# Kernel optimization log

Hardware: AMD Instinct MI355X
Metric: run time of the kernel (lower is better)

Reference implementation:

```python
import jax, jax.numpy as jnp
import numpy as np

B, L, D = 8, 2048, 512
H, P = 8, 4
C = D // H  # dim_per_head


def setup_inputs() -> dict:
    key = jax.random.key(0)
    ks = jax.random.split(key, 11)
    sc = lambda k, shape, s=0.02: jax.random.normal(k, shape, jnp.float32) * s
    return dict(
        query=jax.random.normal(ks[0], (B, L, D), jnp.float32),
        key_in=jax.random.normal(ks[1], (B, L, D), jnp.float32),
        value=jax.random.normal(ks[2], (B, L, D), jnp.float32),
        W_v=sc(ks[3], (D, D)), b_v=jnp.zeros((D,), jnp.float32),
        W_off=sc(ks[4], (D, H * P * 2), 0.01), b_off=sc(ks[5], (H * P * 2,), 0.2),
        W_aw=sc(ks[6], (D, H * P), 0.01), b_aw=jnp.zeros((H * P,), jnp.float32),
        W_out=sc(ks[7], (D, D)), b_out=jnp.zeros((D,), jnp.float32),
    )


def reference(query, key_in, value, W_v, b_v, W_off, b_off, W_aw, b_aw, W_out, b_out):
    # value projection
    v = value @ W_v + b_v                                        # (B,L,D)
    # sampling offsets and attention weights from the query
    off = (query @ W_off + b_off).reshape(B, L, H, P, 2)         # (B,L,H,P,2)
    aw = jax.nn.softmax((query @ W_aw + b_aw).reshape(B, L, H, P), axis=-1)
    # reference point for query i is (x=linspace[0]=0, y=linspace[i]) because
    # the torch code slices reference_points[:, :, :, :1, :]
    ref_y = jnp.linspace(0.0, 1.0, L, dtype=jnp.float32)
    loc_x = jnp.clip(off[..., 0], 0.0, 1.0)                      # ref_x = 0
    loc_y = jnp.clip(off[..., 1] + ref_y[None, :, None, None], 0.0, 1.0)
    # grid_sample, align_corners=False, input (BH, C, 1, L)
    ix = ((loc_x + 1.0) * L - 1.0) * 0.5                         # width coord in [ (L-1)/2, L-0.5 ]
    iy = loc_y * 0.5                                             # ((y+1)*1 - 1)/2
    ix0 = jnp.floor(ix)
    fx = ix - ix0
    iy0 = jnp.floor(iy)
    fy = iy - iy0
    # height dim has size 1: row iy0 valid iff ==0, row iy0+1 valid iff ==0 (zero padding)
    ywt = (1.0 - fy) * (iy0 == 0.0).astype(jnp.float32) + fy * ((iy0 + 1.0) == 0.0).astype(jnp.float32)
    i0 = ix0.astype(jnp.int32)
    i1 = i0 + 1

    perm = lambda a: a.transpose(0, 2, 1, 3)                     # (B,L,H,P) -> (B,H,L,P)
    i0p, i1p = perm(i0), perm(i1)
    vh = v.reshape(B, L, H, C).transpose(0, 2, 1, 3)             # (B,H,L,C)

    gather = jax.vmap(jax.vmap(lambda vm, ii: vm[ii]))           # (L,C),(L,P) -> (L,P,C)
    m0 = ((i0p >= 0) & (i0p < L)).astype(jnp.float32)[..., None]
    m1 = ((i1p >= 0) & (i1p < L)).astype(jnp.float32)[..., None]
    g0 = gather(vh, jnp.clip(i0p, 0, L - 1)) * m0                # (B,H,L,P,C)
    g1 = gather(vh, jnp.clip(i1p, 0, L - 1)) * m1

    fxp = perm(fx)[..., None]
    ywtp = perm(ywt)[..., None]
    samp = ywtp * ((1.0 - fxp) * g0 + fxp * g1)                  # (B,H,L,P,C)
    out = (samp * perm(aw)[..., None]).sum(axis=3)               # (B,H,L,C)
    out = out.transpose(0, 2, 1, 3).reshape(B, L, D)
    return out @ W_out + b_out
```

## Files before the change

### kernel.cpp

```cpp
#include <hip/hip_runtime.h>
#include <stdint.h>

#define PSZF (16384 * 96)

using short8  = __attribute__((ext_vector_type(8))) short;
using floatx4 = __attribute__((ext_vector_type(4))) float;

__device__ __forceinline__ unsigned short f2bf(float f) {
  union { float f; unsigned u; } v; v.f = f;
  unsigned r = v.u + 0x7fffu + ((v.u >> 16) & 1u);
  return (unsigned short)(r >> 16);
}
__device__ __forceinline__ float bf2f(unsigned short u) {
  union { unsigned u; float f; } v; v.u = ((unsigned)u) << 16; return v.f;
}

__device__ __forceinline__ void load_lds16(const void* g, void* l) {
  __builtin_amdgcn_global_load_lds(
      (const __attribute__((address_space(1))) unsigned int*)g,
      (__attribute__((address_space(3))) unsigned int*)l, 16, 0, 0);
}

__device__ __forceinline__ short8 cvt8(float4 a, float4 b) {
  short8 r;
  r[0] = (short)f2bf(a.x); r[1] = (short)f2bf(a.y);
  r[2] = (short)f2bf(a.z); r[3] = (short)f2bf(a.w);
  r[4] = (short)f2bf(b.x); r[5] = (short)f2bf(b.y);
  r[6] = (short)f2bf(b.z); r[7] = (short)f2bf(b.w);
  return r;
}

__global__ __launch_bounds__(256) void prep_all(const float* __restrict__ W_v,
                                                const float* __restrict__ W_out,
                                                const float* __restrict__ Woff,
                                                const float* __restrict__ Waw,
                                                unsigned short* __restrict__ Wv_t,
                                                unsigned short* __restrict__ Wo_t,
                                                unsigned short* __restrict__ Bhi,
                                                unsigned short* __restrict__ Blo) {
  int t = blockIdx.x * 256 + threadIdx.x;
  if (t < 262144) {
    int n = t >> 9, k = t & 511;
    Wv_t[t] = f2bf(W_v[(k << 9) + n]);
    return;
  }
  t -= 262144;
  if (t < 262144) {
    int n = t >> 9, k = t & 511;
    Wo_t[t] = f2bf(W_out[(k << 9) + n]);
    return;
  }
  t -= 262144;
  if (t < 49152) {
    int n = t >> 9, k = t & 511;
    float w = (n < 64) ? Woff[(k << 6) + n] : Waw[(k << 5) + (n - 64)];
    unsigned short hi = f2bf(w);
    Bhi[t] = hi;
    Blo[t] = f2bf(w - bf2f(hi));
  }
}

__device__ __forceinline__ void gemm_body64_bf16A(unsigned char* smem,
                                                  const unsigned short* __restrict__ A,
                                                  const unsigned short* __restrict__ Bt,
                                                  const float* __restrict__ bias,
                                                  float* __restrict__ C, int bx, int by) {
  unsigned short* lA = (unsigned short*)smem;
  unsigned short* lB = (unsigned short*)(smem + 16384);
  int tid  = threadIdx.x;
  int lane = tid & 63, wv = tid >> 6;
  int wm = wv & 1, wn = wv >> 1;
  int lrow = lane & 15, quad = lane >> 4;
  int rowBlk = by * 128, colBlk = bx * 128;

  const unsigned short* Ab = A + (size_t)rowBlk * 512;
  const unsigned short* Bb = Bt + (size_t)colBlk * 512;
  int r0 = tid >> 2;
  int c0 = (tid & 3) << 3;

  floatx4 acc[4][4];
#pragma unroll
  for (int i = 0; i < 4; i++)
#pragma unroll
    for (int j = 0; j < 4; j++) acc[i][j] = (floatx4){0.f, 0.f, 0.f, 0.f};

  for (int k0 = 0; k0 < 512; k0 += 64) {
    load_lds16(Ab + (size_t)r0 * 512 + k0 + c0,             lA + tid * 8);
    load_lds16(Ab + (size_t)(r0 + 64) * 512 + k0 + c0,      lA + 2048 + tid * 8);
    load_lds16(Bb + (size_t)r0 * 512 + k0 + c0,             lB + tid * 8);
    load_lds16(Bb + (size_t)(r0 + 64) * 512 + k0 + c0,      lB + 2048 + tid * 8);
    load_lds16(Ab + (size_t)r0 * 512 + k0 + 32 + c0,        lA + 4096 + tid * 8);
    load_lds16(Ab + (size_t)(r0 + 64) * 512 + k0 + 32 + c0, lA + 6144 + tid * 8);
    load_lds16(Bb + (size_t)r0 * 512 + k0 + 32 + c0,        lB + 4096 + tid * 8);
    load_lds16(Bb + (size_t)(r0 + 64) * 512 + k0 + 32 + c0, lB + 6144 + tid * 8);
    __syncthreads();

#pragma unroll
    for (int kc = 0; kc < 2; kc++) {
      short8 a[4], b[4];
#pragma unroll
      for (int mi = 0; mi < 4; mi++)
        a[mi] = *(const short8*)&lA[kc * 4096 + (wm * 64 + mi * 16 + lrow) * 32 + quad * 8];
#pragma unroll
      for (int ni = 0; ni < 4; ni++)
        b[ni] = *(const short8*)&lB[kc * 4096 + (wn * 64 + ni * 16 + lrow) * 32 + quad * 8];
#pragma unroll
      for (int mi = 0; mi < 4; mi++)
#pragma unroll
        for (int ni = 0; ni < 4; ni++)
          acc[mi][ni] = __builtin_amdgcn_mfma_f32_16x16x32_bf16(a[mi], b[ni], acc[mi][ni], 0, 0, 0);
    }
    __syncthreads();
  }

#pragma unroll
  for (int ni = 0; ni < 4; ni++) {
    int col = colBlk + wn * 64 + ni * 16 + lrow;
    float bv = bias[col];
#pragma unroll
    for (int mi = 0; mi < 4; mi++) {
      int row = rowBlk + wm * 64 + mi * 16 + quad * 4;
#pragma unroll
      for (int r = 0; r < 4; r++)
        C[(size_t)(row + r) * 512 + col] = acc[mi][ni][r] + bv;
    }
  }
}

__device__ __forceinline__ void gemm_body64_f32A(unsigned char* smem,
                                                 const float* __restrict__ Af,
                                                 const unsigned short* __restrict__ Bt,
                                                 const float* __restrict__ bias,
                                                 unsigned short* __restrict__ C, int bx, int by) {
  unsigned short* lA = (unsigned short*)smem;
  unsigned short* lB = (unsigned short*)(smem + 16384);
  int tid  = threadIdx.x;
  int lane = tid & 63, wv = tid >> 6;
  int wm = wv & 1, wn = wv >> 1;
  int lrow = lane & 15, quad = lane >> 4;
  int rowBlk = by * 128, colBlk = bx * 128;

  const unsigned short* Bb = Bt + (size_t)colBlk * 512;
  int r0 = tid >> 2;
  int c0 = (tid & 3) << 3;
  const float* Ar0 = Af + (size_t)(rowBlk + r0) * 512 + c0;
  const float* Ar1 = Af + (size_t)(rowBlk + r0 + 64) * 512 + c0;

  floatx4 acc[4][4];
#pragma unroll
  for (int i = 0; i < 4; i++)
#pragma unroll
    for (int j = 0; j < 4; j++) acc[i][j] = (floatx4){0.f, 0.f, 0.f, 0.f};

  float4 a00 = *(const float4*)(Ar0);
  float4 a01 = *(const float4*)(Ar0 + 4);
  float4 a10 = *(const float4*)(Ar1);
  float4 a11 = *(const float4*)(Ar1 + 4);
  float4 a02 = *(const float4*)(Ar0 + 32);
  float4 a03 = *(const float4*)(Ar0 + 36);
  float4 a12 = *(const float4*)(Ar1 + 32);
  float4 a13 = *(const float4*)(Ar1 + 36);

  for (int k0 = 0; k0 < 512; k0 += 64) {
    load_lds16(Bb + (size_t)r0 * 512 + k0 + c0,             lB + tid * 8);
    load_lds16(Bb + (size_t)(r0 + 64) * 512 + k0 + c0,      lB + 2048 + tid * 8);
    load_lds16(Bb + (size_t)r0 * 512 + k0 + 32 + c0,        lB + 4096 + tid * 8);
    load_lds16(Bb + (size_t)(r0 + 64) * 512 + k0 + 32 + c0, lB + 6144 + tid * 8);
    *(short8*)&lA[tid * 8]        = cvt8(a00, a01);
    *(short8*)&lA[2048 + tid * 8] = cvt8(a10, a11);
    *(short8*)&lA[4096 + tid * 8] = cvt8(a02, a03);
    *(short8*)&lA[6144 + tid * 8] = cvt8(a12, a13);
    if (k0 < 448) {
      int kk = k0 + 64;
      a00 = *(const float4*)(Ar0 + kk);
      a01 = *(const float4*)(Ar0 + kk + 4);
      a10 = *(const float4*)(Ar1 + kk);
      a11 = *(const float4*)(Ar1 + kk + 4);
      a02 = *(const float4*)(Ar0 + kk + 32);
      a03 = *(const float4*)(Ar0 + kk + 36);
      a12 = *(const float4*)(Ar1 + kk + 32);
      a13 = *(const float4*)(Ar1 + kk + 36);
      asm volatile("s_waitcnt vmcnt(8)" ::: "memory");
    } else {
      asm volatile("s_waitcnt vmcnt(0)" ::: "memory");
    }
    asm volatile("s_waitcnt lgkmcnt(0)" ::: "memory");
    __builtin_amdgcn_sched_barrier(0);
    __builtin_amdgcn_s_barrier();
    __builtin_amdgcn_sched_barrier(0);

#pragma unroll
    for (int kc = 0; kc < 2; kc++) {
      short8 a[4], b[4];
#pragma unroll
      for (int mi = 0; mi < 4; mi++)
        a[mi] = *(const short8*)&lA[kc * 4096 + (wm * 64 + mi * 16 + lrow) * 32 + quad * 8];
#pragma unroll
      for (int ni = 0; ni < 4; ni++)
        b[ni] = *(const short8*)&lB[kc * 4096 + (wn * 64 + ni * 16 + lrow) * 32 + quad * 8];
#pragma unroll
      for (int mi = 0; mi < 4; mi++)
#pragma unroll
        for (int ni = 0; ni < 4; ni++)
          acc[mi][ni] = __builtin_amdgcn_mfma_f32_16x16x32_bf16(a[mi], b[ni], acc[mi][ni], 0, 0, 0);
    }
    __builtin_amdgcn_sched_barrier(0);
    __builtin_amdgcn_s_barrier();
  }

#pragma unroll
  for (int ni = 0; ni < 4; ni++) {
    int col = colBlk + wn * 64 + ni * 16 + lrow;
    float bv = bias[col];
#pragma unroll
    for (int mi = 0; mi < 4; mi++) {
      int row = rowBlk + wm * 64 + mi * 16 + quad * 4;
#pragma unroll
      for (int r = 0; r < 4; r++)
        C[(size_t)(row + r) * 512 + col] = f2bf(acc[mi][ni][r] + bv);
    }
  }
}

__device__ __forceinline__ void swz512(int bid, int& bx, int& by) {
  int x = bid & 7, s = bid >> 3;
  by = (x << 4) | (s >> 2);
  bx = s & 3;
}

__device__ __forceinline__ void offaw_body(unsigned char* smem,
                                           const float* __restrict__ Q,
                                           const unsigned short* __restrict__ Bhi,
                                           const unsigned short* __restrict__ Blo,
                                           const float* __restrict__ boff,
                                           const float* __restrict__ baw,
                                           float* __restrict__ P, int bid) {
  unsigned short* lAhi = (unsigned short*)smem;
  unsigned short* lAlo = (unsigned short*)(smem + 4096);
  unsigned short* lBhi = (unsigned short*)(smem + 8192);
  unsigned short* lBlo = (unsigned short*)(smem + 14336);
  int khalf = bid >> 8, row0 = (bid & 255) * 64, kbase = khalf << 8;
  int tid = threadIdx.x, lane = tid & 63, wv = tid >> 6;
  int wm = wv & 1, wn = wv >> 1, lrow = lane & 15, quad = lane >> 4;

  int ar = tid >> 2, ac = (tid & 3) << 3;
  const float* qp = Q + (size_t)(row0 + ar) * 512 + kbase + ac;

  floatx4 acc[2][3];
#pragma unroll
  for (int i = 0; i < 2; i++)
#pragma unroll
    for (int j = 0; j < 3; j++) acc[i][j] = (floatx4){0.f, 0.f, 0.f, 0.f};

  float4 v0 = *(const float4*)(qp);
  float4 v1 = *(const float4*)(qp + 4);

  for (int k0 = 0; k0 < 256; k0 += 32) {
#pragma unroll
    for (int j = 0; j < 3; j++) {
      int widx = wv + (j << 2);
      const unsigned short* src = (widx < 6) ? Bhi : Blo;
      unsigned short* dst = (widx < 6) ? lBhi : lBlo;
      int c = (((widx < 6) ? widx : widx - 6) << 6) + lane;
      int n = c >> 2, cc = (c & 3) << 3;
      load_lds16(src + (size_t)n * 512 + kbase + k0 + cc, dst + c * 8);
    }
    {
      float vv[8] = {v0.x, v0.y, v0.z, v0.w, v1.x, v1.y, v1.z, v1.w};
      short8 h8, l8;
#pragma unroll
      for (int e = 0; e < 8; e++) {
        union { float f; unsigned u; } t; t.f = vv[e];
        unsigned r = t.u + 0x7fffu + ((t.u >> 16) & 1u);
        h8[e] = (short)(r >> 16);
        union { unsigned u; float f; } hf; hf.u = r & 0xffff0000u;
        union { float f; unsigned u; } rb; rb.f = vv[e] - hf.f;
        l8[e] = (short)(rb.u >> 16);
      }
      *(short8*)&lAhi[tid * 8] = h8;
      *(short8*)&lAlo[tid * 8] = l8;
    }
    if (k0 < 224) {
      v0 = *(const float4*)(qp + k0 + 32);
      v1 = *(const float4*)(qp + k0 + 36);
      asm volatile("s_waitcnt vmcnt(2)" ::: "memory");
    } else {
      asm volatile("s_waitcnt vmcnt(0)" ::: "memory");
    }
    asm volatile("s_waitcnt lgkmcnt(0)" ::: "memory");
    __builtin_amdgcn_sched_barrier(0);
    __builtin_amdgcn_s_barrier();
    __builtin_amdgcn_sched_barrier(0);

    short8 ah[2], al[2], bh[3], bl[3];
#pragma unroll
    for (int mi = 0; mi < 2; mi++) {
      int r = (wm * 32 + mi * 16 + lrow) * 32 + quad * 8;
      ah[mi] = *(const short8*)&lAhi[r];
      al[mi] = *(const short8*)&lAlo[r];
    }
#pragma unroll
    for (int ni = 0; ni < 3; ni++) {
      int r = (wn * 48 + ni * 16 + lrow) * 32 + quad * 8;
      bh[ni] = *(const short8*)&lBhi[r];
      bl[ni] = *(const short8*)&lBlo[r];
    }
#pragma unroll
    for (int mi = 0; mi < 2; mi++)
#pragma unroll
      for (int ni = 0; ni < 3; ni++) {
        acc[mi][ni] = __builtin_amdgcn_mfma_f32_16x16x32_bf16(ah[mi], bh[ni], acc[mi][ni], 0, 0, 0);
        acc[mi][ni] = __builtin_amdgcn_mfma_f32_16x16x32_bf16(ah[mi], bl[ni], acc[mi][ni], 0, 0, 0);
        acc[mi][ni] = __builtin_amdgcn_mfma_f32_16x16x32_bf16(al[mi], bh[ni], acc[mi][ni], 0, 0, 0);
      }
    __builtin_amdgcn_sched_barrier(0);
    __builtin_amdgcn_s_barrier();
  }

  float* out = P + (size_t)khalf * PSZF;
#pragma unroll
  for (int ni = 0; ni < 3; ni++) {
    int col = wn * 48 + ni * 16 + lrow;
    float bv = (khalf == 0) ? ((col < 64) ? boff[col] : baw[col - 64]) : 0.0f;
#pragma unroll
    for (int mi = 0; mi < 2; mi++) {
      int row = row0 + wm * 32 + mi * 16 + quad * 4;
#pragma unroll
      for (int r = 0; r < 4; r++)
        out[(size_t)(row + r) * 96 + col] = acc[mi][ni][r] + bv;
    }
  }
}

__global__ __launch_bounds__(256) void mega_k1(const float* __restrict__ value,
                                               const unsigned short* __restrict__ Wv_t,
                                               const float* __restrict__ b_v,
                                               unsigned short* __restrict__ v_bf,
                                               const float* __restrict__ query,
                                               const unsigned short* __restrict__ Bhi,
                                               const unsigned short* __restrict__ Blo,
                                               const float* __restrict__ boff,
                                               const float* __restrict__ baw,
                                               float* __restrict__ offP) {
  __shared__ __align__(16) unsigned char smem[32768];
  int bid = blockIdx.x;
  if (bid < 512) {
    int bx, by; swz512(bid, bx, by);
    gemm_body64_f32A(smem, value, Wv_t, b_v, v_bf, bx, by);
  } else {
    offaw_body(smem, query, Bhi, Blo, boff, baw, offP, bid - 512);
  }
}

__global__ __launch_bounds__(256) void gemm2_k(const unsigned short* __restrict__ A,
                                               const unsigned short* __restrict__ Bt,
                                               const float* __restrict__ bias,
                                               float* __restrict__ C) {
  __shared__ __align__(16) unsigned char smem[32768];
  int bx, by; swz512(blockIdx.x, bx, by);
  gemm_body64_bf16A(smem, A, Bt, bias, C, bx, by);
}

__global__ __launch_bounds__(256) void sample_kernel(const float* __restrict__ P,
                                                     const unsigned short* __restrict__ v,
                                                     unsigned short* __restrict__ attn) {
  int tid = threadIdx.x;
  int rr = tid >> 5, hp = tid & 31;
  int row = blockIdx.x * 8 + rr;
  int l = row & 2047;
  __shared__ float s_w0[8][32], s_w1[8][32];
  __shared__ int s_i0[8][32], s_i1[8][32];
  {
    int base = row * 96;
    float lg = P[base + 64 + hp] + P[PSZF + base + 64 + hp];
    float mx = fmaxf(lg, __shfl_xor(lg, 1));
    mx = fmaxf(mx, __shfl_xor(mx, 2));
    float e = __expf(lg - mx);
    float s = e + __shfl_xor(e, 1);
    s = s + __shfl_xor(s, 2);
    float aw = e / s;

    float ox = P[base + 2 * hp] + P[PSZF + base + 2 * hp];
    float oy = P[base + 2 * hp + 1] + P[PSZF + base + 2 * hp + 1];
    float refy = (float)l * (1.0f / 2047.0f);
    float lx = fminf(fmaxf(ox, 0.0f), 1.0f);
    float ly = fminf(fmaxf(oy + refy, 0.0f), 1.0f);
    float ix = ((lx + 1.0f) * 2048.0f - 1.0f) * 0.5f;
    float ywt = 1.0f - ly * 0.5f;
    float ix0 = floorf(ix);
    float fx = ix - ix0;
    int i0 = (int)ix0;
    int i1 = i0 + 1;
    s_w0[rr][hp] = aw * ywt * (1.0f - fx);
    s_w1[rr][hp] = (i1 < 2048) ? (aw * ywt * fx) : 0.0f;
    s_i0[rr][hp] = i0;
    s_i1[rr][hp] = (i1 < 2048) ? i1 : 2047;
  }
  __syncthreads();

  int b = (blockIdx.x * 8) >> 11;
  int h = tid >> 5, c = (tid & 31) << 1;
  const unsigned short* vhc = v + ((size_t)(b << 11)) * 512 + h * 64 + c;
#pragma unroll
  for (int r8 = 0; r8 < 8; r8++) {
    int row2 = blockIdx.x * 8 + r8;
    float ax = 0.0f, ay = 0.0f;
#pragma unroll
    for (int p = 0; p < 4; p++) {
      int t = (h << 2) + p;
      unsigned g0 = *(const unsigned*)(vhc + ((size_t)s_i0[r8][t] << 9));
      unsigned g1 = *(const unsigned*)(vhc + ((size_t)s_i1[r8][t] << 9));
      float w0 = s_w0[r8][t], w1 = s_w1[r8][t];
      ax += w0 * bf2f((unsigned short)g0) + w1 * bf2f((unsigned short)g1);
      ay += w0 * bf2f((unsigned short)(g0 >> 16)) + w1 * bf2f((unsigned short)(g1 >> 16));
    }
    unsigned packed = (unsigned)f2bf(ax) | ((unsigned)f2bf(ay) << 16);
    *(unsigned*)(attn + (size_t)row2 * 512 + h * 64 + c) = packed;
  }
}

extern "C" void kernel_launch(void* const* d_in, const int* in_sizes, int n_in,
                              void* d_out, int out_size, void* d_ws, size_t ws_size,
                              hipStream_t stream) {
  (void)in_sizes; (void)n_in; (void)out_size; (void)ws_size;
  const float* query = (const float*)d_in[0];
  const float* value = (const float*)d_in[2];
  const float* W_v   = (const float*)d_in[3];
  const float* b_v   = (const float*)d_in[4];
  const float* W_off = (const float*)d_in[5];
  const float* b_off = (const float*)d_in[6];
  const float* W_aw  = (const float*)d_in[7];
  const float* b_aw  = (const float*)d_in[8];
  const float* W_out = (const float*)d_in[9];
  const float* b_out = (const float*)d_in[10];
  float* out = (float*)d_out;

  char* ws = (char*)d_ws;
  const size_t MB = 1ull << 20;
  unsigned short* attn   = (unsigned short*)(ws);
  unsigned short* v_bf   = (unsigned short*)(ws + 16 * MB);
  float* offP            = (float*)(ws + 32 * MB);
  unsigned short* Wv_t   = (unsigned short*)(ws + 48 * MB);
  unsigned short* Wo_t   = (unsigned short*)(ws + 48 * MB + 524288);
  unsigned short* Bhi    = (unsigned short*)(ws + 49 * MB);
  unsigned short* Blo    = (unsigned short*)(ws + 49 * MB + 98304);

  prep_all<<<2240, 256, 0, stream>>>(W_v, W_out, W_off, W_aw, Wv_t, Wo_t, Bhi, Blo);
  mega_k1<<<1024, 256, 0, stream>>>(value, Wv_t, b_v, v_bf, query, Bhi, Blo,
                                    b_off, b_aw, offP);
  sample_kernel<<<2048, 256, 0, stream>>>(offP, v_bf, attn);
  gemm2_k<<<512, 256, 0, stream>>>(attn, Wo_t, b_out, out);
}
```

Baseline: 190.2 us.

## Replace LDS-staged GEMM tiles with direct global-to-register MFMA operand loads

```diff
diff --git a/kernel.cpp b/kernel.cpp
--- a/kernel.cpp
+++ b/kernel.cpp
@@ -60,23 +60,20 @@
   }
 }
 
-__device__ __forceinline__ void gemm_body64_bf16A(unsigned char* smem,
-                                                  const unsigned short* __restrict__ A,
-                                                  const unsigned short* __restrict__ Bt,
-                                                  const float* __restrict__ bias,
-                                                  float* __restrict__ C, int bx, int by) {
-  unsigned short* lA = (unsigned short*)smem;
-  unsigned short* lB = (unsigned short*)(smem + 16384);
-  int tid  = threadIdx.x;
+__device__ __forceinline__ void gemm_reg_f32A(const float* __restrict__ Af,
+                                              const unsigned short* __restrict__ Bt,
+                                              const float* __restrict__ bias,
+                                              unsigned short* __restrict__ C,
+                                              int bx, int by) {
+  int tid = threadIdx.x;
   int lane = tid & 63, wv = tid >> 6;
   int wm = wv & 1, wn = wv >> 1;
   int lrow = lane & 15, quad = lane >> 4;
-  int rowBlk = by * 128, colBlk = bx * 128;
-
-  const unsigned short* Ab = A + (size_t)rowBlk * 512;
-  const unsigned short* Bb = Bt + (size_t)colBlk * 512;
-  int r0 = tid >> 2;
-  int c0 = (tid & 3) << 3;
+  int row0 = by * 128 + wm * 64;
+  int col0 = bx * 128 + wn * 64;
+
+  const float* Ab = Af + (size_t)(row0 + lrow) * 512 + quad * 8;
+  const unsigned short* Bb = Bt + (size_t)(col0 + lrow) * 512 + quad * 8;
 
   floatx4 acc[4][4];
 #pragma unroll
@@ -84,67 +81,54 @@
 #pragma unroll
     for (int j = 0; j < 4; j++) acc[i][j] = (floatx4){0.f, 0.f, 0.f, 0.f};
 
-  for (int k0 = 0; k0 < 512; k0 += 64) {
-    load_lds16(Ab + (size_t)r0 * 512 + k0 + c0,             lA + tid * 8);
-    load_lds16(Ab + (size_t)(r0 + 64) * 512 + k0 + c0,      lA + 2048 + tid * 8);
-    load_lds16(Bb + (size_t)r0 * 512 + k0 + c0,             lB + tid * 8);
-    load_lds16(Bb + (size_t)(r0 + 64) * 512 + k0 + c0,      lB + 2048 + tid * 8);
-    load_lds16(Ab + (size_t)r0 * 512 + k0 + 32 + c0,        lA + 4096 + tid * 8);
-    load_lds16(Ab + (size_t)(r0 + 64) * 512 + k0 + 32 + c0, lA + 6144 + tid * 8);
-    load_lds16(Bb + (size_t)r0 * 512 + k0 + 32 + c0,        lB + 4096 + tid * 8);
-    load_lds16(Bb + (size_t)(r0 + 64) * 512 + k0 + 32 + c0, lB + 6144 + tid * 8);
-    __syncthreads();
-
-#pragma unroll
-    for (int kc = 0; kc < 2; kc++) {
-      short8 a[4], b[4];
-#pragma unroll
-      for (int mi = 0; mi < 4; mi++)
-        a[mi] = *(const short8*)&lA[kc * 4096 + (wm * 64 + mi * 16 + lrow) * 32 + quad * 8];
+#pragma unroll 2
+  for (int k0 = 0; k0 < 512; k0 += 32) {
+    short8 a[4], b[4];
+#pragma unroll
+    for (int mi = 0; mi < 4; mi++) {
+      const float* ap = Ab + (size_t)mi * 16 * 512 + k0;
+      float4 lo = *(const float4*)(ap);
+      float4 hi = *(const float4*)(ap + 4);
+      a[mi] = cvt8(lo, hi);
+    }
+#pragma unroll
+    for (int ni = 0; ni < 4; ni++)
+      b[ni] = *(const short8*)(Bb + (size_t)ni * 16 * 512 + k0);
+#pragma unroll
+    for (int mi = 0; mi < 4; mi++)
 #pragma unroll
       for (int ni = 0; ni < 4; ni++)
-        b[ni] = *(const short8*)&lB[kc * 4096 + (wn * 64 + ni * 16 + lrow) * 32 + quad * 8];
-#pragma unroll
-      for (int mi = 0; mi < 4; mi++)
-#pragma unroll
-        for (int ni = 0; ni < 4; ni++)
-          acc[mi][ni] = __builtin_amdgcn_mfma_f32_16x16x32_bf16(a[mi], b[ni], acc[mi][ni], 0, 0, 0);
-    }
-    __syncthreads();
+        acc[mi][ni] = __builtin_amdgcn_mfma_f32_16x16x32_bf16(a[mi], b[ni], acc[mi][ni], 0, 0, 0);
   }
 
 #pragma unroll
   for (int ni = 0; ni < 4; ni++) {
-    int col = colBlk + wn * 64 + ni * 16 + lrow;
+    int col = col0 + ni * 16 + lrow;
     float bv = bias[col];
 #pragma unroll
     for (int mi = 0; mi < 4; mi++) {
-      int row = rowBlk + wm * 64 + mi * 16 + quad * 4;
+      int row = row0 + mi * 16 + quad * 4;
 #pragma unroll
       for (int r = 0; r < 4; r++)
-        C[(size_t)(row + r) * 512 + col] = acc[mi][ni][r] + bv;
-    }
-  }
-}
-
-__device__ __forceinline__ void gemm_body64_f32A(unsigned char* smem,
-                                                 const float* __restrict__ Af,
-                                                 const unsigned short* __restrict__ Bt,
-                                                 const float* __restrict__ bias,
-                                                 unsigned short* __restrict__ C, int bx, int by) {
-  unsigned short* lA = (unsigned short*)smem;
-  unsigned short* lB = (unsigned short*)(smem + 16384);
-  int tid  = threadIdx.x;
+        C[(size_t)(row + r) * 512 + col] = f2bf(acc[mi][ni][r] + bv);
+    }
+  }
+}
+
+__device__ __forceinline__ void gemm_reg_bf16A(const unsigned short* __restrict__ A,
+                                               const unsigned short* __restrict__ Bt,
+                                               const float* __restrict__ bias,
+                                               float* __restrict__ C,
+                                               int bx, int by) {
+  int tid = threadIdx.x;
   int lane = tid & 63, wv = tid >> 6;
   int wm = wv & 1, wn = wv >> 1;
   int lrow = lane & 15, quad = lane >> 4;
-  int rowBlk = by * 128, colBlk = bx * 128;
-
-  const unsigned short* Bb = Bt + (size_t)colBlk * 512;
-  int r0 = tid >> 2;
-  int c0 = (tid & 3) << 3;
-  const float* Ar0 = Af + (size_t)(rowBlk + r0) * 512 + c0;
-  const float* Ar1 = Af + (size_t)(rowBlk + r0 + 64) * 512 + c0;
+  int row0 = by * 128 + wm * 64;
+  int col0 = bx * 128 + wn * 64;
+
+  const unsigned short* Ab = A + (size_t)(row0 + lrow) * 512 + quad * 8;
+  const unsigned short* Bb = Bt + (size_t)(col0 + lrow) * 512 + quad * 8;
 
   floatx4 acc[4][4];
 #pragma unroll
@@ -152,72 +136,32 @@
 #pragma unroll
     for (int j = 0; j < 4; j++) acc[i][j] = (floatx4){0.f, 0.f, 0.f, 0.f};
 
-  float4 a00 = *(const float4*)(Ar0);
-  float4 a01 = *(const float4*)(Ar0 + 4);
-  float4 a10 = *(const float4*)(Ar1);
-  float4 a11 = *(const float4*)(Ar1 + 4);
-  float4 a02 = *(const float4*)(Ar0 + 32);
-  float4 a03 = *(const float4*)(Ar0 + 36);
-  float4 a12 = *(const float4*)(Ar1 + 32);
-  float4 a13 = *(const float4*)(Ar1 + 36);
-
-  for (int k0 = 0; k0 < 512; k0 += 64) {
-    load_lds16(Bb + (size_t)r0 * 512 + k0 + c0,             lB + tid * 8);
-    load_lds16(Bb + (size_t)(r0 + 64) * 512 + k0 + c0,      lB + 2048 + tid * 8);
-    load_lds16(Bb + (size_t)r0 * 512 + k0 + 32 + c0,        lB + 4096 + tid * 8);
-    load_lds16(Bb + (size_t)(r0 + 64) * 512 + k0 + 32 + c0, lB + 6144 + tid * 8);
-    *(short8*)&lA[tid * 8]        = cvt8(a00, a01);
-    *(short8*)&lA[2048 + tid * 8] = cvt8(a10, a11);
-    *(short8*)&lA[4096 + tid * 8] = cvt8(a02, a03);
-    *(short8*)&lA[6144 + tid * 8] = cvt8(a12, a13);
-    if (k0 < 448) {
-      int kk = k0 + 64;
-      a00 = *(const float4*)(Ar0 + kk);
-      a01 = *(const float4*)(Ar0 + kk + 4);
-      a10 = *(const float4*)(Ar1 + kk);
-      a11 = *(const float4*)(Ar1 + kk + 4);
-      a02 = *(const float4*)(Ar0 + kk + 32);
-      a03 = *(const float4*)(Ar0 + kk + 36);
-      a12 = *(const float4*)(Ar1 + kk + 32);
-      a13 = *(const float4*)(Ar1 + kk + 36);
-      asm volatile("s_waitcnt vmcnt(8)" ::: "memory");
-    } else {
-      asm volatile("s_waitcnt vmcnt(0)" ::: "memory");
-    }
-    asm volatile("s_waitcnt lgkmcnt(0)" ::: "memory");
-    __builtin_amdgcn_sched_barrier(0);
-    __builtin_amdgcn_s_barrier();
-    __builtin_amdgcn_sched_barrier(0);
-
-#pragma unroll
-    for (int kc = 0; kc < 2; kc++) {
-      short8 a[4], b[4];
-#pragma unroll
-      for (int mi = 0; mi < 4; mi++)
-        a[mi] = *(const short8*)&lA[kc * 4096 + (wm * 64 + mi * 16 + lrow) * 32 + quad * 8];
+#pragma unroll 4
+  for (int k0 = 0; k0 < 512; k0 += 32) {
+    short8 a[4], b[4];
+#pragma unroll
+    for (int mi = 0; mi < 4; mi++)
+      a[mi] = *(const short8*)(Ab + (size_t)mi * 16 * 512 + k0);
+#pragma unroll
+    for (int ni = 0; ni < 4; ni++)
+      b[ni] = *(const short8*)(Bb + (size_t)ni * 16 * 512 + k0);
+#pragma unroll
+    for (int mi = 0; mi < 4; mi++)
 #pragma unroll
       for (int ni = 0; ni < 4; ni++)
-        b[ni] = *(const short8*)&lB[kc * 4096 + (wn * 64 + ni * 16 + lrow) * 32 + quad * 8];
-#pragma unroll
-      for (int mi = 0; mi < 4; mi++)
-#pragma unroll
-        for (int ni = 0; ni < 4; ni++)
-          acc[mi][ni] = __builtin_amdgcn_mfma_f32_16x16x32_bf16(a[mi], b[ni], acc[mi][ni], 0, 0, 0);
-    }
-    __builtin_amdgcn_sched_barrier(0);
-    __builtin_amdgcn_s_barrier();
+        acc[mi][ni] = __builtin_amdgcn_mfma_f32_16x16x32_bf16(a[mi], b[ni], acc[mi][ni], 0, 0, 0);
   }
 
 #pragma unroll
   for (int ni = 0; ni < 4; ni++) {
-    int col = colBlk + wn * 64 + ni * 16 + lrow;
+    int col = col0 + ni * 16 + lrow;
     float bv = bias[col];
 #pragma unroll
     for (int mi = 0; mi < 4; mi++) {
-      int row = rowBlk + wm * 64 + mi * 16 + quad * 4;
+      int row = row0 + mi * 16 + quad * 4;
 #pragma unroll
       for (int r = 0; r < 4; r++)
-        C[(size_t)(row + r) * 512 + col] = f2bf(acc[mi][ni][r] + bv);
+        C[(size_t)(row + r) * 512 + col] = acc[mi][ni][r] + bv;
     }
   }
 }
@@ -342,11 +286,11 @@
                                                const float* __restrict__ boff,
                                                const float* __restrict__ baw,
                                                float* __restrict__ offP) {
-  __shared__ __align__(16) unsigned char smem[32768];
+  __shared__ __align__(16) unsigned char smem[20480];
   int bid = blockIdx.x;
   if (bid < 512) {
     int bx, by; swz512(bid, bx, by);
-    gemm_body64_f32A(smem, value, Wv_t, b_v, v_bf, bx, by);
+    gemm_reg_f32A(value, Wv_t, b_v, v_bf, bx, by);
   } else {
     offaw_body(smem, query, Bhi, Blo, boff, baw, offP, bid - 512);
   }
@@ -356,9 +300,8 @@
                                                const unsigned short* __restrict__ Bt,
                                                const float* __restrict__ bias,
                                                float* __restrict__ C) {
-  __shared__ __align__(16) unsigned char smem[32768];
   int bx, by; swz512(blockIdx.x, bx, by);
-  gemm_body64_bf16A(smem, A, Bt, bias, C, bx, by);
+  gemm_reg_bf16A(A, Bt, bias, C, bx, by);
 }
 
 __global__ __launch_bounds__(256) void sample_kernel(const float* __restrict__ P,
```

After: 236.1 us. 1.24x slower.
